# Optimization experiments

Measured on AMD Instinct MI355X. Metric: run time of the kernel, lower is better.

The kernel has to match this reference:

```python
import jax, jax.numpy as jnp
import numpy as np


def _fft(x_real, x_imag):
    # Recursive radix-2 Cooley-Tukey, decimation in time.
    # N is static (256), so the recursion fully unrolls at trace time.
    N = x_real.shape[-1]
    if N == 1:
        return x_real, x_imag
    even_real, even_imag = _fft(x_real[..., ::2], x_imag[..., ::2])
    odd_real, odd_imag = _fft(x_real[..., 1::2], x_imag[..., 1::2])
    k = jnp.arange(N // 2, dtype=jnp.float32).reshape(1, -1)
    angle = -2.0 * jnp.pi * k / float(N)
    cos = jnp.cos(angle)
    sin = jnp.sin(angle)
    t_real = cos * odd_real - sin * odd_imag
    t_imag = cos * odd_imag + sin * odd_real
    real = jnp.concatenate([even_real + t_real, even_real - t_real], axis=-1)
    imag = jnp.concatenate([even_imag + t_imag, even_imag - t_imag], axis=-1)
    return real, imag


def setup_inputs() -> dict:
    key = jax.random.key(0)
    x = jax.random.normal(key, (131072, 2, 256), dtype=jnp.float32)
    return {"x": x}


def reference(x):
    # x: [B, 2, 256] (real/imag channels)
    real, imag = _fft(x[:, 0, :], x[:, 1, :])
    return jnp.stack([real, imag], axis=1)
```

## Files before the change

### kernel.cpp

```cpp
#include <hip/hip_runtime.h>
#include <math.h>


#define NB 16

__device__ __forceinline__ void fft16(float re[16], float im[16]) {
    {
        float tr, ti;
#define SWP(a, b) tr = re[a]; re[a] = re[b]; re[b] = tr; ti = im[a]; im[a] = im[b]; im[b] = ti;
        SWP(1, 8) SWP(2, 4) SWP(3, 12) SWP(5, 10) SWP(7, 14) SWP(11, 13)
#undef SWP
    }
    const float C[8] = { 1.0f,  0.92387953251f,  0.70710678119f,  0.38268343236f,
                         0.0f, -0.38268343236f, -0.70710678119f, -0.92387953251f };
    const float S[8] = { 0.0f, -0.38268343236f, -0.70710678119f, -0.92387953251f,
                        -1.0f, -0.92387953251f, -0.70710678119f, -0.38268343236f };
#pragma unroll
    for (int s = 1; s <= 4; ++s) {
        const int len = 1 << s;
        const int half = len >> 1;
        const int step = 16 >> s;
#pragma unroll
        for (int i = 0; i < 16; i += len) {
#pragma unroll
            for (int j = 0; j < half; ++j) {
                const float wr = C[j * step];
                const float wi = S[j * step];
                const int p = i + j;
                const int q = i + j + half;
                const float vr = re[q] * wr - im[q] * wi;
                const float vi = re[q] * wi + im[q] * wr;
                const float ur = re[p], ui = im[p];
                re[p] = ur + vr; im[p] = ui + vi;
                re[q] = ur - vr; im[q] = ui - vi;
            }
        }
    }
}

__global__ __launch_bounds__(256) void fft256_kernel(const float* __restrict__ x,
                                                     float* __restrict__ out) {
    __shared__ float lre[NB][16][17];
    __shared__ float lim[NB][16][17];

    const int tid = threadIdx.x;
    const int sub = tid >> 4;
    const int t   = tid & 15;
    const int b   = blockIdx.x * NB + sub;

    const float* xr = x + (size_t)b * 512;
    const float* xi = xr + 256;

    float re[16], im[16];

#pragma unroll
    for (int i = 0; i < 16; ++i) {
        re[i] = xr[t + 16 * i];
        im[i] = xi[t + 16 * i];
    }

    fft16(re, im);

#pragma unroll
    for (int k = 0; k < 16; ++k) {
        float sv, cv;
        __sincosf(-6.283185307179586f * (float)(t * k) * (1.0f / 256.0f), &sv, &cv);
        lre[sub][t][k] = re[k] * cv - im[k] * sv;
        lim[sub][t][k] = re[k] * sv + im[k] * cv;
    }

    __syncthreads();

#pragma unroll
    for (int n = 0; n < 16; ++n) {
        re[n] = lre[sub][n][t];
        im[n] = lim[sub][n][t];
    }

    fft16(re, im);

    float* outr = out + (size_t)b * 512;
    float* outi = outr + 256;
#pragma unroll
    for (int k = 0; k < 16; ++k) {
        outr[t + 16 * k] = re[k];
        outi[t + 16 * k] = im[k];
    }
}

extern "C" void kernel_launch(void* const* d_in, const int* in_sizes, int n_in,
                              void* d_out, int out_size, void* d_ws, size_t ws_size,
                              hipStream_t stream) {
    (void)d_ws; (void)ws_size; (void)n_in;
    const float* x = (const float*)d_in[0];
    float* out = (float*)d_out;
    const int batches = in_sizes[0] / 512;
    const int grid = batches / NB;
    fft256_kernel<<<grid, 256, 0, stream>>>(x, out);
}
```

Before: 102.0 us.

## Halve shared memory, replace block barrier with wave barriers, use nontemporal IO

Each 16-thread FFT group now transposes through a single 272-float shared tile, handling imaginary then real parts one after the other, so shared memory per block is halved. The block-wide __syncthreads is replaced by wave-level barriers, since each group sits inside one wavefront. Global loads and stores become nontemporal, and launch bounds ask for 8 blocks per CU. The aim is higher occupancy and less sync and cache overhead on this streaming, memory-bound kernel, at the cost of two extra LDS round trips and a reliance on wavefront-local execution for correctness.

Measured after the change: 152.8 us. +49.8%, slower.

```diff
diff --git a/kernel.cpp b/kernel.cpp
--- a/kernel.cpp
+++ b/kernel.cpp
@@ -3,6 +3,11 @@
 
 
 #define NB 16
+#define TS 272
+
+__device__ __forceinline__ void wave_fence() {
+    __builtin_amdgcn_wave_barrier();
+}
 
 __device__ __forceinline__ void fft16(float re[16], float im[16]) {
     {
@@ -13,8 +18,8 @@
     }
     const float C[8] = { 1.0f,  0.92387953251f,  0.70710678119f,  0.38268343236f,
                          0.0f, -0.38268343236f, -0.70710678119f, -0.92387953251f };
-    const float S[8] = { 0.0f, -0.38268343236f, -0.70710678119f, -0.92387953251f,
-                        -1.0f, -0.92387953251f, -0.70710678119f, -0.38268343236f };
+    const float S16[8] = { 0.0f, -0.38268343236f, -0.70710678119f, -0.92387953251f,
+                          -1.0f, -0.92387953251f, -0.70710678119f, -0.38268343236f };
 #pragma unroll
     for (int s = 1; s <= 4; ++s) {
         const int len = 1 << s;
@@ -25,7 +30,7 @@
 #pragma unroll
             for (int j = 0; j < half; ++j) {
                 const float wr = C[j * step];
-                const float wi = S[j * step];
+                const float wi = S16[j * step];
                 const int p = i + j;
                 const int q = i + j + half;
                 const float vr = re[q] * wr - im[q] * wi;
@@ -38,60 +43,64 @@
     }
 }
 
-__global__ __launch_bounds__(256) void fft256_kernel(const float* __restrict__ x,
-                                                     float* __restrict__ out) {
-    __shared__ float lre[NB][16][17];
-    __shared__ float lim[NB][16][17];
+__global__ __launch_bounds__(256, 8) void fft256_kernel(const float* __restrict__ x,
+                                                        float* __restrict__ out) {
+    __shared__ float tile[NB * TS];
 
     const int tid = threadIdx.x;
     const int sub = tid >> 4;
     const int t   = tid & 15;
-    const int b   = blockIdx.x * NB + sub;
+    const long b  = (long)blockIdx.x * NB + sub;
 
-    const float* xr = x + (size_t)b * 512;
+    const float* xr = x + b * 512;
     const float* xi = xr + 256;
 
     float re[16], im[16];
 
 #pragma unroll
-    for (int i = 0; i < 16; ++i) {
-        re[i] = xr[t + 16 * i];
-        im[i] = xi[t + 16 * i];
-    }
+    for (int i = 0; i < 16; ++i) re[i] = __builtin_nontemporal_load(xr + t + 16 * i);
+#pragma unroll
+    for (int i = 0; i < 16; ++i) im[i] = __builtin_nontemporal_load(xi + t + 16 * i);
 
     fft16(re, im);
+
+    float* L = tile + sub * TS;
 
 #pragma unroll
     for (int k = 0; k < 16; ++k) {
         float sv, cv;
         __sincosf(-6.283185307179586f * (float)(t * k) * (1.0f / 256.0f), &sv, &cv);
-        lre[sub][t][k] = re[k] * cv - im[k] * sv;
-        lim[sub][t][k] = re[k] * sv + im[k] * cv;
+        const float tr = re[k] * cv - im[k] * sv;
+        const float ti = re[k] * sv + im[k] * cv;
+        L[17 * t + k] = ti;
+        re[k] = tr;
     }
-
-    __syncthreads();
+    wave_fence();
 
 #pragma unroll
-    for (int n = 0; n < 16; ++n) {
-        re[n] = lre[sub][n][t];
-        im[n] = lim[sub][n][t];
-    }
+    for (int n = 0; n < 16; ++n) im[n] = L[17 * n + t];
+    wave_fence();
+
+#pragma unroll
+    for (int k = 0; k < 16; ++k) L[17 * t + k] = re[k];
+    wave_fence();
+#pragma unroll
+    for (int n = 0; n < 16; ++n) re[n] = L[17 * n + t];
 
     fft16(re, im);
 
-    float* outr = out + (size_t)b * 512;
+    float* outr = out + b * 512;
     float* outi = outr + 256;
 #pragma unroll
-    for (int k = 0; k < 16; ++k) {
-        outr[t + 16 * k] = re[k];
-        outi[t + 16 * k] = im[k];
-    }
+    for (int k = 0; k < 16; ++k) __builtin_nontemporal_store(re[k], outr + t + 16 * k);
+#pragma unroll
+    for (int k = 0; k < 16; ++k) __builtin_nontemporal_store(im[k], outi + t + 16 * k);
 }
 
 extern "C" void kernel_launch(void* const* d_in, const int* in_sizes, int n_in,
                               void* d_out, int out_size, void* d_ws, size_t ws_size,
                               hipStream_t stream) {
-    (void)d_ws; (void)ws_size; (void)n_in;
+    (void)d_ws; (void)ws_size; (void)n_in; (void)out_size;
     const float* x = (const float*)d_in[0];
     float* out = (float*)d_out;
     const int batches = in_sizes[0] / 512;
```
